# Optimization experiments

Measured on AMD Instinct MI355X. Metric: run time of the kernel, lower is better.

Reference implementation:

```python
import jax, jax.numpy as jnp
import numpy as np

MARKET_DIM, VELOCITY_DIM, AGENT_STATE_DIM = 20, 10, 10
RUNNER_DIM, POSITION_DIM, MAX_RUNNERS = 24, 8, 30
RUNNER_INPUT_DIM = RUNNER_DIM + POSITION_DIM            # 32
MARKET_TOTAL_DIM = MARKET_DIM + VELOCITY_DIM + AGENT_STATE_DIM  # 40
OBS_DIM = MARKET_DIM + VELOCITY_DIM + MAX_RUNNERS * RUNNER_DIM + AGENT_STATE_DIM + MAX_RUNNERS * POSITION_DIM  # 1000
TD_IDX = MARKET_DIM + (VELOCITY_DIM - 4)                # 26
B, T = 256, 64
MLP_H, LSTM_H = 128, 256
LSTM_IN = MLP_H + 2 * MLP_H                             # 384


def setup_inputs() -> dict:
    key = jax.random.key(0)
    ks = jax.random.split(key, 32)

    def w(k, o, i):
        return (jax.random.normal(k, (o, i), jnp.float32) / np.sqrt(i)).astype(jnp.float32)

    z = lambda n: jnp.zeros((n,), jnp.float32)
    return dict(
        obs=jax.random.normal(ks[0], (B, T, OBS_DIM), jnp.float32),
        # runner encoder: 32 -> 128 -> 128 -> 128
        re_w0=w(ks[1], MLP_H, RUNNER_INPUT_DIM), re_b0=z(MLP_H),
        re_w1=w(ks[2], MLP_H, MLP_H), re_b1=z(MLP_H),
        re_w2=w(ks[3], MLP_H, MLP_H), re_b2=z(MLP_H),
        # market encoder: 40 -> 128 -> 128 -> 128
        me_w0=w(ks[4], MLP_H, MARKET_TOTAL_DIM), me_b0=z(MLP_H),
        me_w1=w(ks[5], MLP_H, MLP_H), me_b1=z(MLP_H),
        me_w2=w(ks[6], MLP_H, MLP_H), me_b2=z(MLP_H),
        # TimeLSTM cell (single layer)
        W_ih=w(ks[7], 4 * LSTM_H, LSTM_IN), b_ih=z(4 * LSTM_H),
        W_hh=w(ks[8], 4 * LSTM_H, LSTM_H),
        W_dt=jnp.zeros((LSTM_H,), jnp.float32),
        # actor head: 384 -> 128 -> 2
        a_w0=w(ks[9], MLP_H, MLP_H + LSTM_H), a_b0=z(MLP_H),
        a_w1=w(ks[10], 2, MLP_H) * 0.01, a_b1=z(2),
        # critic head: 256 -> 128 -> 1
        c_w0=w(ks[11], MLP_H, LSTM_H), c_b0=z(MLP_H),
        c_w1=w(ks[12], 1, MLP_H), c_b1=z(1),
        log_std=jnp.zeros((MAX_RUNNERS * 2,), jnp.float32),
    )


def _mlp3(x, w0, b0, w1, b1, w2, b2):
    x = jax.nn.relu(x @ w0.T + b0)
    x = jax.nn.relu(x @ w1.T + b1)
    return x @ w2.T + b2


def _mlp2(x, w0, b0, w1, b1):
    return jax.nn.relu(x @ w0.T + b0) @ w1.T + b1


def reference(obs,
              re_w0, re_b0, re_w1, re_b1, re_w2, re_b2,
              me_w0, me_b0, me_w1, me_b1, me_w2, me_b2,
              W_ih, b_ih, W_hh, W_dt,
              a_w0, a_b0, a_w1, a_b1,
              c_w0, c_b0, c_w1, c_b1,
              log_std):
    b, t, _ = obs.shape
    of = obs.reshape(b * t, -1)
    market = of[:, :MARKET_DIM]
    vel = of[:, MARKET_DIM:MARKET_DIM + VELOCITY_DIM]
    rs = MARKET_DIM + VELOCITY_DIM
    re_ = rs + MAX_RUNNERS * RUNNER_DIM
    runners = of[:, rs:re_].reshape(b * t, MAX_RUNNERS, RUNNER_DIM)
    agent = of[:, re_:re_ + AGENT_STATE_DIM]
    ps = re_ + AGENT_STATE_DIM
    pos = of[:, ps:ps + MAX_RUNNERS * POSITION_DIM].reshape(b * t, MAX_RUNNERS, POSITION_DIM)

    market_feats = jnp.concatenate([market, vel, agent], axis=-1)        # (BT, 40)
    runner_feats = jnp.concatenate([runners, pos], axis=-1)              # (BT, R, 32)

    market_emb = _mlp3(market_feats, me_w0, me_b0, me_w1, me_b1, me_w2, me_b2)  # (BT, 128)
    runner_embs = _mlp3(runner_feats, re_w0, re_b0, re_w1, re_b1, re_w2, re_b2)  # (BT, R, 128)
    r_mean = runner_embs.mean(axis=1)
    r_max = runner_embs.max(axis=1)

    lstm_in = jnp.concatenate([market_emb, r_mean, r_max], axis=-1).reshape(b, t, LSTM_IN)
    dt = of[:, TD_IDX].reshape(b, t)

    h0 = jnp.zeros((b, LSTM_H), obs.dtype)
    c0 = jnp.zeros_like(h0)

    def step(hc, xs):
        h, c = hc
        x, d = xs                                           # (B, 384), (B,)
        gates = x @ W_ih.T + b_ih + h @ W_hh.T              # (B, 4H)
        i, f, g, o = jnp.split(gates, 4, axis=-1)
        f = f + W_dt * d[:, None]                           # time-modulated forget gate
        i, f, o = jax.nn.sigmoid(i), jax.nn.sigmoid(f), jax.nn.sigmoid(o)
        g = jnp.tanh(g)
        c_new = f * c + i * g
        h_new = o * jnp.tanh(c_new)
        return (h_new, c_new), None

    (h, c), _ = jax.lax.scan(step, (h0, c0), (lstm_in.transpose(1, 0, 2), dt.T))
    lstm_out = h  # layer_norm disabled -> identity

    runner_last = runner_embs.reshape(b, t, MAX_RUNNERS, MLP_H)[:, -1]   # (B, R, 128)
    actor_in = jnp.concatenate(
        [runner_last, jnp.broadcast_to(lstm_out[:, None, :], (b, MAX_RUNNERS, LSTM_H))], axis=-1)
    action_mean = _mlp2(actor_in, a_w0, a_b0, a_w1, a_b1).reshape(b, MAX_RUNNERS * 2)
    action_log_std = jnp.broadcast_to(log_std, action_mean.shape)
    value = _mlp2(lstm_out, c_w0, c_b0, c_w1, c_b1)                      # (B, 1)
    return action_mean, action_log_std, value, h, c
```

## Files before the change

### kernel.cpp

```cpp
#include <hip/hip_runtime.h>
#include <hip/hip_bf16.h>
#include <math.h>

#define Bn 256
#define Tn 64
#define OBSD 1000
#define NR 30
#define HD 128
#define LH 256
#define LIN 384
#define TDI 26

#define AM_OFF 0
#define ALS_OFF 15360
#define V_OFF 30720
#define H_OFF 30976
#define C_OFF 96512

typedef unsigned short u16;
typedef short bf16x8 __attribute__((ext_vector_type(8)));
typedef float f32x4 __attribute__((ext_vector_type(4)));

__device__ __forceinline__ float sigm(float x){ return 1.f/(1.f+__expf(-x)); }
__device__ __forceinline__ float tanhfast(float x){
    float ax = fabsf(x);
    float e = __expf(2.f*ax);
    float t = 1.f - 2.f/(e+1.f);
    return copysignf(t, x);
}

__device__ __forceinline__ u16 f2b(float f){
    union { __hip_bfloat16 h; u16 u; } cv;
    cv.h = __float2bfloat16(f);
    return cv.u;
}

__device__ __forceinline__ bf16x8 ld_b128_sys(const u16* p){
    bf16x8 r;
    asm volatile("global_load_dwordx4 %0, %1, off sc0 sc1"
                 : "=v"(r) : "v"(p) : "memory");
    return r;
}
__device__ __forceinline__ void st_b16_sys(u16* p, unsigned v){
    asm volatile("global_store_short %0, %1, off sc0 sc1"
                 :: "v"(p), "v"(v) : "memory");
}

#define MFMA(a,b,c) __builtin_amdgcn_mfma_f32_16x16x32_bf16(a,b,c,0,0,0)

__device__ __forceinline__ void pack_one(
    const float* __restrict__ src, u16* __restrict__ dst,
    int N, int K, int Kpad, int t)
{
    if (t >= N*Kpad) return;
    int j = t / Kpad, k = t - j*Kpad;
    float v = (k < K) ? src[j*K + k] : 0.f;
    int ntile = j>>4, jr = j&15, kc = k>>5, ko = k&31;
    int lane = ((ko>>3)<<4) | jr, elem = ko&7;
    int KC = Kpad>>5;
    dst[(size_t)(((ntile*KC + kc)*64) + lane)*8 + elem] = f2b(v);
}

__device__ __forceinline__ void pack_gi_one(
    const float* __restrict__ src, u16* __restrict__ dst, int K, int t)
{
    int KC = K >> 5;
    if (t >= 1024*K) return;
    int n = t / K, k = t - n*K;
    int nt = n>>4, jr = n&15;
    int jg = nt>>2, g = nt&3;
    float v = src[(size_t)(g*256 + jg*16 + jr)*K + k];
    int kc = k>>5, ko = k&31;
    int lane = ((ko>>3)<<4) | jr, e = ko&7;
    dst[(size_t)(((nt*KC + kc)*64) + lane)*8 + e] = f2b(v);
}

__global__ __launch_bounds__(256) void k_setup(
    const float* __restrict__ re_w0, u16* __restrict__ pw0,
    const float* __restrict__ re_w1, u16* __restrict__ pw1,
    const float* __restrict__ re_w2, u16* __restrict__ pw2,
    const float* __restrict__ me_w0, u16* __restrict__ pm0,
    const float* __restrict__ me_w1, u16* __restrict__ pm1,
    const float* __restrict__ me_w2, u16* __restrict__ pm2,
    const float* __restrict__ W_ih,  u16* __restrict__ pwih,
    const float* __restrict__ W_hh,  u16* __restrict__ pwhh,
    const float* __restrict__ obs,   float* __restrict__ dtv)
{
    int blk = blockIdx.x, tid = threadIdx.x;
    if (blk < 16){            pack_one(re_w0, pw0, 128, 32, 32,  blk*256 + tid); }
    else if (blk < 80){       pack_one(re_w1, pw1, 128,128,128, (blk-16)*256 + tid); }
    else if (blk < 144){      pack_one(re_w2, pw2, 128,128,128, (blk-80)*256 + tid); }
    else if (blk < 176){      pack_one(me_w0, pm0, 128, 40, 64, (blk-144)*256 + tid); }
    else if (blk < 240){      pack_one(me_w1, pm1, 128,128,128, (blk-176)*256 + tid); }
    else if (blk < 304){      pack_one(me_w2, pm2, 128,128,128, (blk-240)*256 + tid); }
    else if (blk < 1840){     pack_gi_one(W_ih, pwih, 384, (blk-304)*256 + tid); }
    else if (blk < 2864){     pack_gi_one(W_hh, pwhh, 256, (blk-1840)*256 + tid); }
    else {
        int idx = (blk-2864)*256 + tid;
        int b = idx >> 6, t = idx & 63;
        dtv[t*256 + b] = obs[(size_t)idx*OBSD + TDI];
    }
}

__global__ __launch_bounds__(256) void k_embed_market(
    const float* __restrict__ obs,
    const u16* __restrict__ pw0, const float* __restrict__ re_b0,
    const u16* __restrict__ pw1, const float* __restrict__ re_b1,
    const u16* __restrict__ pw2, const float* __restrict__ re_b2,
    const u16* __restrict__ pm0, const float* __restrict__ me_b0,
    const u16* __restrict__ pm1, const float* __restrict__ me_b1,
    const u16* __restrict__ pm2, const float* __restrict__ me_b2,
    u16* __restrict__ li_bf, float* __restrict__ runner_last)
{
    __shared__ __align__(16) u16 smem[19968];
    __shared__ float bsf[384];

    int blk = blockIdx.x, tid = threadIdx.x;
    int lane = tid & 63, wv = tid >> 6;
    int lr = lane & 15, lk = lane >> 4;
    f32x4 zero = {0.f,0.f,0.f,0.f};

    if (blk < 8192){
        u16* xr   = smem;
        u16* act1 = smem + 2560;
        u16* act2 = smem + 11264;
        float* bs0 = bsf, *bs1 = bsf+128, *bs2 = bsf+256;

        int bt0 = blk*2;

        for (int idx=tid; idx<2048; idx+=256){
            int r = idx>>5, k = idx&31;
            int sb = r>>5, rr = r&31;
            const float* row = obs + (size_t)(bt0+sb)*OBSD;
            float v = 0.f;
            if (rr < 30) v = (k<24) ? row[30 + rr*24 + k] : row[760 + rr*8 + (k-24)];
            xr[r*40 + k] = f2b(v);
        }
        if (tid < 128){ bs0[tid]=re_b0[tid]; bs1[tid]=re_b1[tid]; bs2[tid]=re_b2[tid]; }
        __syncthreads();

        f32x4 d[4][2];

        {
            bf16x8 a0[4];
            #pragma unroll
            for (int m=0;m<4;m++) a0[m] = *(const bf16x8*)(xr + (m*16+lr)*40 + lk*8);
            #pragma unroll
            for (int ns=0; ns<2; ns++){
                int n = 2*wv + ns;
                bf16x8 b = *(const bf16x8*)(pw0 + (size_t)(n*64 + lane)*8);
                #pragma unroll
                for (int m=0;m<4;m++) d[m][ns] = MFMA(a0[m], b, zero);
            }
        }
        #pragma unroll
        for (int m=0;m<4;m++)
            #pragma unroll
            for (int ns=0;ns<2;ns++){
                int col = (2*wv+ns)*16 + lr;
                float bias = bs0[col];
                #pragma unroll
                for (int r=0;r<4;r++)
                    act1[(m*16+lk*4+r)*136 + col] = f2b(fmaxf(d[m][ns][r] + bias, 0.f));
            }
        __syncthreads();

        #pragma unroll
        for (int m=0;m<4;m++)
            #pragma unroll
            for (int ns=0;ns<2;ns++) d[m][ns] = zero;
        #pragma unroll
        for (int kc=0; kc<4; kc++){
            bf16x8 am[4];
            #pragma unroll
            for (int m=0;m<4;m++) am[m] = *(const bf16x8*)(act1 + (m*16+lr)*136 + kc*32 + lk*8);
            #pragma unroll
            for (int ns=0; ns<2; ns++){
                int n = 2*wv + ns;
                bf16x8 b = *(const bf16x8*)(pw1 + (size_t)((n*4 + kc)*64 + lane)*8);
                #pragma unroll
                for (int m=0;m<4;m++) d[m][ns] = MFMA(am[m], b, d[m][ns]);
            }
        }
        #pragma unroll
        for (int m=0;m<4;m++)
            #pragma unroll
            for (int ns=0;ns<2;ns++){
                int col = (2*wv+ns)*16 + lr;
                float bias = bs1[col];
                #pragma unroll
                for (int r=0;r<4;r++)
                    act2[(m*16+lk*4+r)*136 + col] = f2b(fmaxf(d[m][ns][r] + bias, 0.f));
            }
        __syncthreads();

        #pragma unroll
        for (int m=0;m<4;m++)
            #pragma unroll
            for (int ns=0;ns<2;ns++) d[m][ns] = zero;
        #pragma unroll
        for (int kc=0; kc<4; kc++){
            bf16x8 am[4];
            #pragma unroll
            for (int m=0;m<4;m++) am[m] = *(const bf16x8*)(act2 + (m*16+lr)*136 + kc*32 + lk*8);
            #pragma unroll
            for (int ns=0; ns<2; ns++){
                int n = 2*wv + ns;
                bf16x8 b = *(const bf16x8*)(pw2 + (size_t)((n*4 + kc)*64 + lane)*8);
                #pragma unroll
                for (int m=0;m<4;m++) d[m][ns] = MFMA(am[m], b, d[m][ns]);
            }
        }

        u16* li0 = li_bf + (size_t)bt0*LIN;
        u16* li1 = li_bf + (size_t)(bt0+1)*LIN;
        bool last1 = (((bt0+1) & 63) == 63);
        int bb1 = (bt0+1) >> 6;

        #pragma unroll
        for (int ns=0; ns<2; ns++){
            int col = (2*wv+ns)*16 + lr;
            float bias = bs2[col];
            float vals[4][4];
            float s0=0.f, m0=-3.4e38f, s1=0.f, m1=-3.4e38f;
            #pragma unroll
            for (int m=0;m<4;m++)
                #pragma unroll
                for (int r=0;r<4;r++){
                    int rw = m*16 + lk*4 + r;
                    float v = d[m][ns][r] + bias;
                    vals[m][r] = v;
                    if (m < 2){
                        bool ok = rw < 30;
                        s0 += ok ? v : 0.f;
                        m0 = fmaxf(m0, ok ? v : -3.4e38f);
                    } else {
                        bool ok = (rw-32) < 30;
                        s1 += ok ? v : 0.f;
                        m1 = fmaxf(m1, ok ? v : -3.4e38f);
                    }
                }
            s0 += __shfl_xor(s0, 16); s0 += __shfl_xor(s0, 32);
            m0 = fmaxf(m0, __shfl_xor(m0, 16)); m0 = fmaxf(m0, __shfl_xor(m0, 32));
            s1 += __shfl_xor(s1, 16); s1 += __shfl_xor(s1, 32);
            m1 = fmaxf(m1, __shfl_xor(m1, 16)); m1 = fmaxf(m1, __shfl_xor(m1, 32));
            if (lk == 0){
                li0[128 + col] = f2b(s0 * (1.0f/30.0f));
                li0[256 + col] = f2b(m0);
            }
            if (lk == 1){
                li1[128 + col] = f2b(s1 * (1.0f/30.0f));
                li1[256 + col] = f2b(m1);
            }
            if (last1){
                #pragma unroll
                for (int m=2;m<4;m++)
                    #pragma unroll
                    for (int r=0;r<4;r++){
                        int rw = m*16 + lk*4 + r - 32;
                        if (rw < 30) runner_last[(size_t)bb1*3840 + rw*128 + col] = vals[m][r];
                    }
            }
        }
    } else {
        u16* xm  = smem;
        u16* ma1 = smem + 2304;
        u16* ma2 = smem + 6656;
        float* bs0 = bsf, *bs1 = bsf+128, *bs2 = bsf+256;

        int bt0 = (blk - 8192)*32;
        for (int idx=tid; idx<2048; idx+=256){
            int r = idx>>6, k = idx&63;
            const float* row = obs + (size_t)(bt0+r)*OBSD;
            float v = 0.f;
            if (k < 30) v = row[k];
            else if (k < 40) v = row[720 + k];
            xm[r*72 + k] = f2b(v);
        }
        if (tid < 128){ bs0[tid]=me_b0[tid]; bs1[tid]=me_b1[tid]; bs2[tid]=me_b2[tid]; }
        __syncthreads();

        f32x4 d[2][2];

        #pragma unroll
        for (int m=0;m<2;m++)
            #pragma unroll
            for (int ns=0;ns<2;ns++) d[m][ns] = zero;
        #pragma unroll
        for (int kc=0; kc<2; kc++){
            bf16x8 a0 = *(const bf16x8*)(xm + lr*72      + kc*32 + lk*8);
            bf16x8 a1 = *(const bf16x8*)(xm + (16+lr)*72 + kc*32 + lk*8);
            #pragma unroll
            for (int ns=0; ns<2; ns++){
                int n = 2*wv + ns;
                bf16x8 b = *(const bf16x8*)(pm0 + (size_t)((n*2 + kc)*64 + lane)*8);
                d[0][ns] = MFMA(a0, b, d[0][ns]);
                d[1][ns] = MFMA(a1, b, d[1][ns]);
            }
        }
        #pragma unroll
        for (int m=0;m<2;m++)
            #pragma unroll
            for (int ns=0;ns<2;ns++){
                int col = (2*wv+ns)*16 + lr;
                float bias = bs0[col];
                #pragma unroll
                for (int r=0;r<4;r++){
                    int rw = m*16 + lk*4 + r;
                    ma1[rw*136 + col] = f2b(fmaxf(d[m][ns][r] + bias, 0.f));
                }
            }
        __syncthreads();

        #pragma unroll
        for (int m=0;m<2;m++)
            #pragma unroll
            for (int ns=0;ns<2;ns++) d[m][ns] = zero;
        #pragma unroll
        for (int kc=0; kc<4; kc++){
            bf16x8 a0 = *(const bf16x8*)(ma1 + lr*136      + kc*32 + lk*8);
            bf16x8 a1 = *(const bf16x8*)(ma1 + (16+lr)*136 + kc*32 + lk*8);
            #pragma unroll
            for (int ns=0; ns<2; ns++){
                int n = 2*wv + ns;
                bf16x8 b = *(const bf16x8*)(pm1 + (size_t)((n*4 + kc)*64 + lane)*8);
                d[0][ns] = MFMA(a0, b, d[0][ns]);
                d[1][ns] = MFMA(a1, b, d[1][ns]);
            }
        }
        #pragma unroll
        for (int m=0;m<2;m++)
            #pragma unroll
            for (int ns=0;ns<2;ns++){
                int col = (2*wv+ns)*16 + lr;
                float bias = bs1[col];
                #pragma unroll
                for (int r=0;r<4;r++){
                    int rw = m*16 + lk*4 + r;
                    ma2[rw*136 + col] = f2b(fmaxf(d[m][ns][r] + bias, 0.f));
                }
            }
        __syncthreads();

        #pragma unroll
        for (int m=0;m<2;m++)
            #pragma unroll
            for (int ns=0;ns<2;ns++) d[m][ns] = zero;
        #pragma unroll
        for (int kc=0; kc<4; kc++){
            bf16x8 a0 = *(const bf16x8*)(ma2 + lr*136      + kc*32 + lk*8);
            bf16x8 a1 = *(const bf16x8*)(ma2 + (16+lr)*136 + kc*32 + lk*8);
            #pragma unroll
            for (int ns=0; ns<2; ns++){
                int n = 2*wv + ns;
                bf16x8 b = *(const bf16x8*)(pm2 + (size_t)((n*4 + kc)*64 + lane)*8);
                d[0][ns] = MFMA(a0, b, d[0][ns]);
                d[1][ns] = MFMA(a1, b, d[1][ns]);
            }
        }
        #pragma unroll
        for (int m=0;m<2;m++)
            #pragma unroll
            for (int ns=0;ns<2;ns++){
                int col = (2*wv+ns)*16 + lr;
                float bias = bs2[col];
                #pragma unroll
                for (int r=0;r<4;r++){
                    int rw = m*16 + lk*4 + r;
                    li_bf[(size_t)(bt0+rw)*LIN + col] = f2b(d[m][ns][r] + bias);
                }
            }
    }
}

__global__ __launch_bounds__(256) void k_xw(
    const u16* __restrict__ A, const u16* __restrict__ pwih,
    const float* __restrict__ b_ih, float* __restrict__ xw)
{
    __shared__ __align__(16) u16 bsh[48*512];

    int tid = threadIdx.x;
    int lane = tid & 63, wv = tid >> 6;
    int lr = lane & 15, lk = lane >> 4;
    int r0 = blockIdx.x*128 + wv*32;

    bf16x8 a[2][12];
    #pragma unroll
    for (int m=0;m<2;m++)
        #pragma unroll
        for (int kc=0;kc<12;kc++)
            a[m][kc] = *(const bf16x8*)(A + (size_t)(r0+m*16+lr)*384 + kc*32 + lk*8);

    for (int jg=0; jg<16; jg++){
        {
            const bf16x8* src = (const bf16x8*)(pwih + (size_t)jg*48*512);
            bf16x8* dst = (bf16x8*)bsh;
            #pragma unroll
            for (int i=0;i<12;i++)
                dst[tid + i*256] = src[tid + i*256];
        }
        __syncthreads();

        f32x4 acc[2][4];
        #pragma unroll
        for (int g=0; g<4; g++){
            float bias = b_ih[g*256 + jg*16 + lr];
            f32x4 v = {bias,bias,bias,bias};
            acc[0][g]=v; acc[1][g]=v;
        }
        #pragma unroll
        for (int kc=0; kc<12; kc++){
            bf16x8 b0 = *(const bf16x8*)(bsh + (size_t)((0*12+kc)*64+lane)*8);
            bf16x8 b1 = *(const bf16x8*)(bsh + (size_t)((1*12+kc)*64+lane)*8);
            bf16x8 b2 = *(const bf16x8*)(bsh + (size_t)((2*12+kc)*64+lane)*8);
            bf16x8 b3 = *(const bf16x8*)(bsh + (size_t)((3*12+kc)*64+lane)*8);
            #pragma unroll
            for (int m=0;m<2;m++){
                acc[m][0] = MFMA(a[m][kc], b0, acc[m][0]);
                acc[m][1] = MFMA(a[m][kc], b1, acc[m][1]);
                acc[m][2] = MFMA(a[m][kc], b2, acc[m][2]);
                acc[m][3] = MFMA(a[m][kc], b3, acc[m][3]);
            }
        }
        #pragma unroll
        for (int m=0;m<2;m++)
            #pragma unroll
            for (int r=0;r<4;r++){
                int row = r0 + m*16 + lk*4 + r;
                int trow = (row & 63)*256 + (row >> 6);
                float4 pk;
                pk.x = acc[m][0][r]; pk.y = acc[m][1][r];
                pk.z = acc[m][2][r]; pk.w = acc[m][3][r];
                *(float4*)(xw + ((size_t)trow*256 + jg*16 + lr)*4) = pk;
            }
        __syncthreads();
    }
}

__global__ __launch_bounds__(256,1) void k_lstm_pair(
    const float* __restrict__ xw, const u16* __restrict__ pwhh,
    const float* __restrict__ W_dt, const float* __restrict__ dtv,
    u16* __restrict__ hb0, u16* __restrict__ hb1,
    float* __restrict__ hout, float* __restrict__ cout,
    unsigned int* __restrict__ flags)
{
    int tid = threadIdx.x;
    int lane = tid & 63, wv = tid >> 6;
    int lr = lane & 15, lk = lane >> 4;
    int blk = blockIdx.x;
    int p = blk >> 1, hf = blk & 1;
    int bb0 = p*16;
    int jg0 = hf*8 + wv*2;

    bf16x8 bfr[2][4][8];
    #pragma unroll
    for (int jl=0;jl<2;jl++)
        #pragma unroll
        for (int g=0;g<4;g++)
            #pragma unroll
            for (int kc=0;kc<8;kc++)
                bfr[jl][g][kc] = *(const bf16x8*)(pwhh + (size_t)((((jg0+jl)*4+g)*8+kc)*64+lane)*8);

    float wdt0 = W_dt[jg0*16 + lr];
    float wdt1 = W_dt[(jg0+1)*16 + lr];

    float cst[2][4] = {{0.f,0.f,0.f,0.f},{0.f,0.f,0.f,0.f}};
    bf16x8 a[8];
    #pragma unroll
    for (int kc=0;kc<8;kc++) a[kc] = (bf16x8)(short)0;

    int bth = bb0 + lk*4;

    float4 xwn[2][4];
    #pragma unroll
    for (int jl=0;jl<2;jl++)
        #pragma unroll
        for (int r=0;r<4;r++)
            xwn[jl][r] = *(const float4*)(xw + ((size_t)(bth+r)*256 + (jg0+jl)*16 + lr)*4);
    float4 dtn = *(const float4*)(dtv + bth);

    unsigned int* myflag   = &flags[blk*64];
    unsigned int* partflag = &flags[(blk^1)*64];

    for (int t=0; t<64; t++){
        asm volatile("s_waitcnt vmcnt(0)" ::: "memory");
        __builtin_amdgcn_sched_barrier(0);

        f32x4 acc[2][4];
        #pragma unroll
        for (int jl=0;jl<2;jl++){
            f32x4 v0, v1, v2, v3;
            #pragma unroll
            for (int r=0;r<4;r++){
                v0[r] = xwn[jl][r].x; v1[r] = xwn[jl][r].y;
                v2[r] = xwn[jl][r].z; v3[r] = xwn[jl][r].w;
            }
            acc[jl][0] = v0; acc[jl][1] = v1; acc[jl][2] = v2; acc[jl][3] = v3;
        }

        #pragma unroll
        for (int kc=0; kc<8; kc++){
            #pragma unroll
            for (int jl=0;jl<2;jl++){
                acc[jl][0] = MFMA(a[kc], bfr[jl][0][kc], acc[jl][0]);
                acc[jl][1] = MFMA(a[kc], bfr[jl][1][kc], acc[jl][1]);
                acc[jl][2] = MFMA(a[kc], bfr[jl][2][kc], acc[jl][2]);
                acc[jl][3] = MFMA(a[kc], bfr[jl][3][kc], acc[jl][3]);
            }
        }

        u16* hw = (t&1) ? hb1 : hb0;
        #pragma unroll
        for (int jl=0;jl<2;jl++){
            float wdt = jl ? wdt1 : wdt0;
            int jcol = (jg0+jl)*16 + lr;
            #pragma unroll
            for (int r=0;r<4;r++){
                float dd = (r==0)?dtn.x:(r==1)?dtn.y:(r==2)?dtn.z:dtn.w;
                float gi = sigm(acc[jl][0][r]);
                float gf = sigm(acc[jl][1][r] + wdt*dd);
                float gg = tanhfast(acc[jl][2][r]);
                float go = sigm(acc[jl][3][r]);
                float cn = fmaf(gf, cst[jl][r], gi*gg);
                cst[jl][r] = cn;
                float hv = go * tanhfast(cn);
                if (t < 63){
                    st_b16_sys(hw + (size_t)(bth+r)*256 + jcol, (unsigned)f2b(hv));
                } else {
                    hout[(size_t)(bth+r)*256 + jcol] = hv;
                    cout[(size_t)(bth+r)*256 + jcol] = cn;
                }
            }
        }

        if (t < 63){
            asm volatile("s_waitcnt vmcnt(0)" ::: "memory");
            __syncthreads();
            if (tid == 0)
                __hip_atomic_store(myflag, (unsigned)(t+1),
                                   __ATOMIC_RELAXED, __HIP_MEMORY_SCOPE_SYSTEM);

            #pragma unroll
            for (int jl=0;jl<2;jl++)
                #pragma unroll
                for (int r=0;r<4;r++)
                    xwn[jl][r] = *(const float4*)(xw + ((size_t)((t+1)*256 + bth+r)*256 + (jg0+jl)*16 + lr)*4);
            dtn = *(const float4*)(dtv + (t+1)*256 + bth);

            if (lane == 0){
                while (__hip_atomic_load(partflag, __ATOMIC_RELAXED,
                                         __HIP_MEMORY_SCOPE_SYSTEM) < (unsigned)(t+1)) {}
            }
            __builtin_amdgcn_wave_barrier();

            const u16* hr = (t&1) ? hb1 : hb0;
            #pragma unroll
            for (int kc=0; kc<8; kc++)
                a[kc] = ld_b128_sys(hr + (size_t)(bb0+lr)*256 + kc*32 + lk*8);
        }
    }
}

__device__ __forceinline__ void dense30(
    const float* in, int istride,
    const float* __restrict__ W, int wstride, int K,
    const float* __restrict__ bias, const float* extra,
    float* outp, int ostride, bool relu, int j, int rh)
{
    float acc[15];
    #pragma unroll
    for (int i=0;i<15;i++) acc[i]=0.f;
    const float* w = W + j*wstride;
    for (int k=0;k<K;k+=4){
        float4 wv = *(const float4*)(w+k);
        #pragma unroll
        for (int i=0;i<15;i++){
            float4 xv = *(const float4*)(in + (rh+2*i)*istride + k);
            acc[i] = fmaf(wv.x,xv.x,acc[i]);
            acc[i] = fmaf(wv.y,xv.y,acc[i]);
            acc[i] = fmaf(wv.z,xv.z,acc[i]);
            acc[i] = fmaf(wv.w,xv.w,acc[i]);
        }
    }
    float bb = bias[j] + (extra ? extra[j] : 0.f);
    #pragma unroll
    for (int i=0;i<15;i++){
        float v = acc[i]+bb;
        outp[(rh+2*i)*ostride+j] = relu ? fmaxf(v,0.f) : v;
    }
}

__device__ __forceinline__ float dense1(
    const float* in, const float* __restrict__ W,
    const float* __restrict__ bias, int K, int j)
{
    const float* w = W + j*K;
    float s = 0.f;
    for (int k=0;k<K;k+=4){
        float4 wv = *(const float4*)(w+k);
        float4 xv = *(const float4*)(in+k);
        s = fmaf(wv.x,xv.x,s); s = fmaf(wv.y,xv.y,s);
        s = fmaf(wv.z,xv.z,s); s = fmaf(wv.w,xv.w,s);
    }
    return s + bias[j];
}

__global__ __launch_bounds__(256) void k_heads(
    const float* __restrict__ h, const float* __restrict__ cbuf,
    const float* __restrict__ rl,
    const float* __restrict__ a_w0, const float* __restrict__ a_b0,
    const float* __restrict__ a_w1, const float* __restrict__ a_b1,
    const float* __restrict__ c_w0, const float* __restrict__ c_b0,
    const float* __restrict__ c_w1, const float* __restrict__ c_b1,
    const float* __restrict__ log_std,
    float* __restrict__ out)
{
    __shared__ __align__(16) float hv[LH];
    __shared__ __align__(16) float rls[NR][HD];
    __shared__ __align__(16) float hid[NR][HD];
    __shared__ __align__(16) float dot2[HD];
    __shared__ __align__(16) float red[128];

    int b = blockIdx.x, tid = threadIdx.x;
    hv[tid] = h[b*LH + tid];
    for (int idx=tid; idx<NR*HD; idx+=256) rls[idx>>7][idx&127] = rl[(size_t)b*NR*HD + idx];
    __syncthreads();

    if (tid < 128){
        const float* w = a_w0 + tid*LIN + HD;
        float s = 0.f;
        for (int k=0;k<LH;k+=4){
            float4 wv = *(const float4*)(w+k);
            s = fmaf(wv.x,hv[k],s); s = fmaf(wv.y,hv[k+1],s);
            s = fmaf(wv.z,hv[k+2],s); s = fmaf(wv.w,hv[k+3],s);
        }
        dot2[tid] = s;
    }
    __syncthreads();

    int j = tid & 127, rh = tid >> 7;
    dense30(&rls[0][0], HD, a_w0, LIN, HD, a_b0, dot2, &hid[0][0], HD, true, j, rh);
    __syncthreads();

    if (tid < 60){
        int r = tid >> 1, o = tid & 1;
        const float* w = a_w1 + o*HD;
        float s = a_b1[o];
        for (int k=0;k<HD;k++) s = fmaf(hid[r][k], w[k], s);
        out[AM_OFF + b*60 + tid] = s;
        out[ALS_OFF + b*60 + tid] = log_std[tid];
    }

    float term = 0.f;
    if (tid < 128) term = fmaxf(dense1(hv, c_w0, c_b0, LH, tid), 0.f) * c_w1[tid];
    if (tid < 128) red[tid] = term;
    __syncthreads();
    for (int s2=64; s2>0; s2>>=1){
        if (tid < s2) red[tid] += red[tid+s2];
        __syncthreads();
    }
    if (tid == 0) out[V_OFF + b] = red[0] + c_b1[0];

    out[H_OFF + b*LH + tid] = hv[tid];
    out[C_OFF + b*LH + tid] = cbuf[b*LH + tid];
}

extern "C" void kernel_launch(void* const* d_in, const int* in_sizes, int n_in,
                              void* d_out, int out_size, void* d_ws, size_t ws_size,
                              hipStream_t stream)
{
    const float* obs   = (const float*)d_in[0];
    const float* re_w0 = (const float*)d_in[1];
    const float* re_b0 = (const float*)d_in[2];
    const float* re_w1 = (const float*)d_in[3];
    const float* re_b1 = (const float*)d_in[4];
    const float* re_w2 = (const float*)d_in[5];
    const float* re_b2 = (const float*)d_in[6];
    const float* me_w0 = (const float*)d_in[7];
    const float* me_b0 = (const float*)d_in[8];
    const float* me_w1 = (const float*)d_in[9];
    const float* me_b1 = (const float*)d_in[10];
    const float* me_w2 = (const float*)d_in[11];
    const float* me_b2 = (const float*)d_in[12];
    const float* W_ih  = (const float*)d_in[13];
    const float* b_ih  = (const float*)d_in[14];
    const float* W_hh  = (const float*)d_in[15];
    const float* W_dt  = (const float*)d_in[16];
    const float* a_w0  = (const float*)d_in[17];
    const float* a_b0  = (const float*)d_in[18];
    const float* a_w1  = (const float*)d_in[19];
    const float* a_b1  = (const float*)d_in[20];
    const float* c_w0  = (const float*)d_in[21];
    const float* c_b0  = (const float*)d_in[22];
    const float* c_w1  = (const float*)d_in[23];
    const float* c_b1  = (const float*)d_in[24];
    const float* lstd  = (const float*)d_in[25];
    float* out = (float*)d_out;

    float* ws = (float*)d_ws;
    size_t off = 0;
    float* xw4  = ws + off; off += (size_t)16384*1024;
    float* hout = ws + off; off += (size_t)Bn*LH;
    float* cb   = ws + off; off += (size_t)Bn*LH;
    float* rl   = ws + off; off += (size_t)Bn*NR*HD;
    float* dtv  = ws + off; off += (size_t)16384;
    unsigned int* flags = (unsigned int*)(ws + off); off += 2048;

    u16* us = (u16*)(ws + off);
    size_t uo = 0;
    u16* li_bf = us + uo; uo += (size_t)16384*LIN;
    u16* pw0   = us + uo; uo += 128*32;
    u16* pw1   = us + uo; uo += 128*128;
    u16* pw2   = us + uo; uo += 128*128;
    u16* pm0   = us + uo; uo += 128*64;
    u16* pm1   = us + uo; uo += 128*128;
    u16* pm2   = us + uo; uo += 128*128;
    u16* pwih  = us + uo; uo += (size_t)1024*384;
    u16* pwhh  = us + uo; uo += (size_t)1024*256;
    u16* hb0   = us + uo; uo += (size_t)Bn*LH;
    u16* hb1   = us + uo; uo += (size_t)Bn*LH;

    hipMemsetAsync(flags, 0, 2048*sizeof(unsigned int), stream);

    k_setup<<<2928, 256, 0, stream>>>(re_w0, pw0, re_w1, pw1, re_w2, pw2,
                                      me_w0, pm0, me_w1, pm1, me_w2, pm2,
                                      W_ih, pwih, W_hh, pwhh, obs, dtv);

    k_embed_market<<<8704, 256, 0, stream>>>(obs,
                                      pw0, re_b0, pw1, re_b1, pw2, re_b2,
                                      pm0, me_b0, pm1, me_b1, pm2, me_b2,
                                      li_bf, rl);

    k_xw<<<128, 256, 0, stream>>>(li_bf, pwih, b_ih, xw4);

    k_lstm_pair<<<32, 256, 0, stream>>>(xw4, pwhh, W_dt, dtv, hb0, hb1,
                                        hout, cb, flags);

    k_heads<<<256, 256, 0, stream>>>(hout, cb, rl,
        a_w0, a_b0, a_w1, a_b1, c_w0, c_b0, c_w1, c_b1, lstd, out);
}
```

Measured before the change: 456.1 us.

## Process four timesteps per runner-embed block, fold flag reset into setup, hoist LSTM acc init

Each runner-encoder block now handles four (b,t) rows instead of two, halving the block count and reusing each weight fragment load across twice as many MFMAs. A single activation buffer is reused across layers, with an extra barrier added. The flag memset is folded into the setup kernel to drop one launch. In the LSTM loop, accumulator initialization from the prefetched xw values moves to the end of the previous iteration so it is off the critical path. The cost is higher register and LDS use per block, which may reduce occupancy.

Measured after the change: 464.6 us. About the same (+1.9%).

```diff
diff --git a/kernel.cpp b/kernel.cpp
--- a/kernel.cpp
+++ b/kernel.cpp
@@ -84,7 +84,8 @@
     const float* __restrict__ me_w2, u16* __restrict__ pm2,
     const float* __restrict__ W_ih,  u16* __restrict__ pwih,
     const float* __restrict__ W_hh,  u16* __restrict__ pwhh,
-    const float* __restrict__ obs,   float* __restrict__ dtv)
+    const float* __restrict__ obs,   float* __restrict__ dtv,
+    unsigned int* __restrict__ flags)
 {
     int blk = blockIdx.x, tid = threadIdx.x;
     if (blk < 16){            pack_one(re_w0, pw0, 128, 32, 32,  blk*256 + tid); }
@@ -95,10 +96,12 @@
     else if (blk < 304){      pack_one(me_w2, pm2, 128,128,128, (blk-240)*256 + tid); }
     else if (blk < 1840){     pack_gi_one(W_ih, pwih, 384, (blk-304)*256 + tid); }
     else if (blk < 2864){     pack_gi_one(W_hh, pwhh, 256, (blk-1840)*256 + tid); }
-    else {
+    else if (blk < 2928){
         int idx = (blk-2864)*256 + tid;
         int b = idx >> 6, t = idx & 63;
         dtv[t*256 + b] = obs[(size_t)idx*OBSD + TDI];
+    } else {
+        flags[(blk-2928)*256 + tid] = 0u;
     }
 }
 
@@ -112,7 +115,7 @@
     const u16* __restrict__ pm2, const float* __restrict__ me_b2,
     u16* __restrict__ li_bf, float* __restrict__ runner_last)
 {
-    __shared__ __align__(16) u16 smem[19968];
+    __shared__ __align__(16) u16 smem[22528];
     __shared__ float bsf[384];
 
     int blk = blockIdx.x, tid = threadIdx.x;
@@ -120,15 +123,14 @@
     int lr = lane & 15, lk = lane >> 4;
     f32x4 zero = {0.f,0.f,0.f,0.f};
 
-    if (blk < 8192){
-        u16* xr   = smem;
-        u16* act1 = smem + 2560;
-        u16* act2 = smem + 11264;
+    if (blk < 4096){
+        u16* xr  = smem;
+        u16* act = smem + 5120;
         float* bs0 = bsf, *bs1 = bsf+128, *bs2 = bsf+256;
 
-        int bt0 = blk*2;
-
-        for (int idx=tid; idx<2048; idx+=256){
+        int bt0 = blk*4;
+
+        for (int idx=tid; idx<4096; idx+=256){
             int r = idx>>5, k = idx&31;
             int sb = r>>5, rr = r&31;
             const float* row = obs + (size_t)(bt0+sb)*OBSD;
@@ -139,126 +141,138 @@
         if (tid < 128){ bs0[tid]=re_b0[tid]; bs1[tid]=re_b1[tid]; bs2[tid]=re_b2[tid]; }
         __syncthreads();
 
-        f32x4 d[4][2];
+        f32x4 d[8][2];
 
         {
-            bf16x8 a0[4];
-            #pragma unroll
-            for (int m=0;m<4;m++) a0[m] = *(const bf16x8*)(xr + (m*16+lr)*40 + lk*8);
+            bf16x8 a0[8];
+            #pragma unroll
+            for (int m=0;m<8;m++) a0[m] = *(const bf16x8*)(xr + (m*16+lr)*40 + lk*8);
             #pragma unroll
             for (int ns=0; ns<2; ns++){
                 int n = 2*wv + ns;
                 bf16x8 b = *(const bf16x8*)(pw0 + (size_t)(n*64 + lane)*8);
                 #pragma unroll
-                for (int m=0;m<4;m++) d[m][ns] = MFMA(a0[m], b, zero);
-            }
-        }
-        #pragma unroll
-        for (int m=0;m<4;m++)
+                for (int m=0;m<8;m++) d[m][ns] = MFMA(a0[m], b, zero);
+            }
+        }
+        #pragma unroll
+        for (int m=0;m<8;m++)
             #pragma unroll
             for (int ns=0;ns<2;ns++){
                 int col = (2*wv+ns)*16 + lr;
                 float bias = bs0[col];
                 #pragma unroll
                 for (int r=0;r<4;r++)
-                    act1[(m*16+lk*4+r)*136 + col] = f2b(fmaxf(d[m][ns][r] + bias, 0.f));
-            }
-        __syncthreads();
-
-        #pragma unroll
-        for (int m=0;m<4;m++)
+                    act[(m*16+lk*4+r)*136 + col] = f2b(fmaxf(d[m][ns][r] + bias, 0.f));
+            }
+        __syncthreads();
+
+        #pragma unroll
+        for (int m=0;m<8;m++)
             #pragma unroll
             for (int ns=0;ns<2;ns++) d[m][ns] = zero;
         #pragma unroll
         for (int kc=0; kc<4; kc++){
-            bf16x8 am[4];
-            #pragma unroll
-            for (int m=0;m<4;m++) am[m] = *(const bf16x8*)(act1 + (m*16+lr)*136 + kc*32 + lk*8);
+            bf16x8 am[8];
+            #pragma unroll
+            for (int m=0;m<8;m++) am[m] = *(const bf16x8*)(act + (m*16+lr)*136 + kc*32 + lk*8);
             #pragma unroll
             for (int ns=0; ns<2; ns++){
                 int n = 2*wv + ns;
                 bf16x8 b = *(const bf16x8*)(pw1 + (size_t)((n*4 + kc)*64 + lane)*8);
                 #pragma unroll
-                for (int m=0;m<4;m++) d[m][ns] = MFMA(am[m], b, d[m][ns]);
-            }
-        }
-        #pragma unroll
-        for (int m=0;m<4;m++)
+                for (int m=0;m<8;m++) d[m][ns] = MFMA(am[m], b, d[m][ns]);
+            }
+        }
+        __syncthreads();
+        #pragma unroll
+        for (int m=0;m<8;m++)
             #pragma unroll
             for (int ns=0;ns<2;ns++){
                 int col = (2*wv+ns)*16 + lr;
                 float bias = bs1[col];
                 #pragma unroll
                 for (int r=0;r<4;r++)
-                    act2[(m*16+lk*4+r)*136 + col] = f2b(fmaxf(d[m][ns][r] + bias, 0.f));
-            }
-        __syncthreads();
-
-        #pragma unroll
-        for (int m=0;m<4;m++)
+                    act[(m*16+lk*4+r)*136 + col] = f2b(fmaxf(d[m][ns][r] + bias, 0.f));
+            }
+        __syncthreads();
+
+        #pragma unroll
+        for (int m=0;m<8;m++)
             #pragma unroll
             for (int ns=0;ns<2;ns++) d[m][ns] = zero;
         #pragma unroll
         for (int kc=0; kc<4; kc++){
-            bf16x8 am[4];
-            #pragma unroll
-            for (int m=0;m<4;m++) am[m] = *(const bf16x8*)(act2 + (m*16+lr)*136 + kc*32 + lk*8);
+            bf16x8 am[8];
+            #pragma unroll
+            for (int m=0;m<8;m++) am[m] = *(const bf16x8*)(act + (m*16+lr)*136 + kc*32 + lk*8);
             #pragma unroll
             for (int ns=0; ns<2; ns++){
                 int n = 2*wv + ns;
                 bf16x8 b = *(const bf16x8*)(pw2 + (size_t)((n*4 + kc)*64 + lane)*8);
                 #pragma unroll
-                for (int m=0;m<4;m++) d[m][ns] = MFMA(am[m], b, d[m][ns]);
-            }
-        }
-
-        u16* li0 = li_bf + (size_t)bt0*LIN;
-        u16* li1 = li_bf + (size_t)(bt0+1)*LIN;
-        bool last1 = (((bt0+1) & 63) == 63);
-        int bb1 = (bt0+1) >> 6;
+                for (int m=0;m<8;m++) d[m][ns] = MFMA(am[m], b, d[m][ns]);
+            }
+        }
+
+        bool last3 = (((bt0+3) & 63) == 63);
+        int bb3 = (bt0+3) >> 6;
 
         #pragma unroll
         for (int ns=0; ns<2; ns++){
             int col = (2*wv+ns)*16 + lr;
             float bias = bs2[col];
-            float vals[4][4];
-            float s0=0.f, m0=-3.4e38f, s1=0.f, m1=-3.4e38f;
-            #pragma unroll
-            for (int m=0;m<4;m++)
+            float vals[8][4];
+            float ss0=0.f, ss1=0.f, ss2=0.f, ss3=0.f;
+            float mm0=-3.4e38f, mm1=-3.4e38f, mm2=-3.4e38f, mm3=-3.4e38f;
+            #pragma unroll
+            for (int m=0;m<8;m++)
                 #pragma unroll
                 for (int r=0;r<4;r++){
                     int rw = m*16 + lk*4 + r;
                     float v = d[m][ns][r] + bias;
                     vals[m][r] = v;
-                    if (m < 2){
-                        bool ok = rw < 30;
-                        s0 += ok ? v : 0.f;
-                        m0 = fmaxf(m0, ok ? v : -3.4e38f);
-                    } else {
-                        bool ok = (rw-32) < 30;
-                        s1 += ok ? v : 0.f;
-                        m1 = fmaxf(m1, ok ? v : -3.4e38f);
-                    }
+                    int sb = m >> 1;
+                    bool ok = (rw - sb*32) < 30;
+                    float va = ok ? v : 0.f;
+                    float vm = ok ? v : -3.4e38f;
+                    if (sb == 0){ ss0 += va; mm0 = fmaxf(mm0, vm); }
+                    else if (sb == 1){ ss1 += va; mm1 = fmaxf(mm1, vm); }
+                    else if (sb == 2){ ss2 += va; mm2 = fmaxf(mm2, vm); }
+                    else { ss3 += va; mm3 = fmaxf(mm3, vm); }
                 }
-            s0 += __shfl_xor(s0, 16); s0 += __shfl_xor(s0, 32);
-            m0 = fmaxf(m0, __shfl_xor(m0, 16)); m0 = fmaxf(m0, __shfl_xor(m0, 32));
-            s1 += __shfl_xor(s1, 16); s1 += __shfl_xor(s1, 32);
-            m1 = fmaxf(m1, __shfl_xor(m1, 16)); m1 = fmaxf(m1, __shfl_xor(m1, 32));
+            ss0 += __shfl_xor(ss0, 16); ss0 += __shfl_xor(ss0, 32);
+            mm0 = fmaxf(mm0, __shfl_xor(mm0, 16)); mm0 = fmaxf(mm0, __shfl_xor(mm0, 32));
+            ss1 += __shfl_xor(ss1, 16); ss1 += __shfl_xor(ss1, 32);
+            mm1 = fmaxf(mm1, __shfl_xor(mm1, 16)); mm1 = fmaxf(mm1, __shfl_xor(mm1, 32));
+            ss2 += __shfl_xor(ss2, 16); ss2 += __shfl_xor(ss2, 32);
+            mm2 = fmaxf(mm2, __shfl_xor(mm2, 16)); mm2 = fmaxf(mm2, __shfl_xor(mm2, 32));
+            ss3 += __shfl_xor(ss3, 16); ss3 += __shfl_xor(ss3, 32);
+            mm3 = fmaxf(mm3, __shfl_xor(mm3, 16)); mm3 = fmaxf(mm3, __shfl_xor(mm3, 32));
             if (lk == 0){
-                li0[128 + col] = f2b(s0 * (1.0f/30.0f));
-                li0[256 + col] = f2b(m0);
-            }
-            if (lk == 1){
-                li1[128 + col] = f2b(s1 * (1.0f/30.0f));
-                li1[256 + col] = f2b(m1);
-            }
-            if (last1){
-                #pragma unroll
-                for (int m=2;m<4;m++)
+                u16* li = li_bf + (size_t)(bt0+0)*LIN;
+                li[128 + col] = f2b(ss0 * (1.0f/30.0f));
+                li[256 + col] = f2b(mm0);
+            } else if (lk == 1){
+                u16* li = li_bf + (size_t)(bt0+1)*LIN;
+                li[128 + col] = f2b(ss1 * (1.0f/30.0f));
+                li[256 + col] = f2b(mm1);
+            } else if (lk == 2){
+                u16* li = li_bf + (size_t)(bt0+2)*LIN;
+                li[128 + col] = f2b(ss2 * (1.0f/30.0f));
+                li[256 + col] = f2b(mm2);
+            } else {
+                u16* li = li_bf + (size_t)(bt0+3)*LIN;
+                li[128 + col] = f2b(ss3 * (1.0f/30.0f));
+                li[256 + col] = f2b(mm3);
+            }
+            if (last3){
+                #pragma unroll
+                for (int m=6;m<8;m++)
                     #pragma unroll
                     for (int r=0;r<4;r++){
-                        int rw = m*16 + lk*4 + r - 32;
-                        if (rw < 30) runner_last[(size_t)bb1*3840 + rw*128 + col] = vals[m][r];
+                        int rwl = m*16 + lk*4 + r - 96;
+                        if (rwl < 30) runner_last[(size_t)bb3*3840 + rwl*128 + col] = vals[m][r];
                     }
             }
         }
@@ -268,7 +282,7 @@
         u16* ma2 = smem + 6656;
         float* bs0 = bsf, *bs1 = bsf+128, *bs2 = bsf+256;
 
-        int bt0 = (blk - 8192)*32;
+        int bt0 = (blk - 4096)*32;
         for (int idx=tid; idx<2048; idx+=256){
             int r = idx>>6, k = idx&63;
             const float* row = obs + (size_t)(bt0+r)*OBSD;
@@ -479,24 +493,24 @@
             xwn[jl][r] = *(const float4*)(xw + ((size_t)(bth+r)*256 + (jg0+jl)*16 + lr)*4);
     float4 dtn = *(const float4*)(dtv + bth);
 
+    f32x4 acc[2][4];
+    #pragma unroll
+    for (int jl=0;jl<2;jl++){
+        f32x4 v0, v1, v2, v3;
+        #pragma unroll
+        for (int r=0;r<4;r++){
+            v0[r] = xwn[jl][r].x; v1[r] = xwn[jl][r].y;
+            v2[r] = xwn[jl][r].z; v3[r] = xwn[jl][r].w;
+        }
+        acc[jl][0] = v0; acc[jl][1] = v1; acc[jl][2] = v2; acc[jl][3] = v3;
+    }
+
     unsigned int* myflag   = &flags[blk*64];
     unsigned int* partflag = &flags[(blk^1)*64];
 
     for (int t=0; t<64; t++){
         asm volatile("s_waitcnt vmcnt(0)" ::: "memory");
         __builtin_amdgcn_sched_barrier(0);
-
-        f32x4 acc[2][4];
-        #pragma unroll
-        for (int jl=0;jl<2;jl++){
-            f32x4 v0, v1, v2, v3;
-            #pragma unroll
-            for (int r=0;r<4;r++){
-                v0[r] = xwn[jl][r].x; v1[r] = xwn[jl][r].y;
-                v2[r] = xwn[jl][r].z; v3[r] = xwn[jl][r].w;
-            }
-            acc[jl][0] = v0; acc[jl][1] = v1; acc[jl][2] = v2; acc[jl][3] = v3;
-        }
 
         #pragma unroll
         for (int kc=0; kc<8; kc++){
@@ -557,6 +571,17 @@
             #pragma unroll
             for (int kc=0; kc<8; kc++)
                 a[kc] = ld_b128_sys(hr + (size_t)(bb0+lr)*256 + kc*32 + lk*8);
+
+            #pragma unroll
+            for (int jl=0;jl<2;jl++){
+                f32x4 v0, v1, v2, v3;
+                #pragma unroll
+                for (int r=0;r<4;r++){
+                    v0[r] = xwn[jl][r].x; v1[r] = xwn[jl][r].y;
+                    v2[r] = xwn[jl][r].z; v3[r] = xwn[jl][r].w;
+                }
+                acc[jl][0] = v0; acc[jl][1] = v1; acc[jl][2] = v2; acc[jl][3] = v3;
+            }
         }
     }
 }
@@ -720,13 +745,11 @@
     u16* hb0   = us + uo; uo += (size_t)Bn*LH;
     u16* hb1   = us + uo; uo += (size_t)Bn*LH;
 
-    hipMemsetAsync(flags, 0, 2048*sizeof(unsigned int), stream);
-
-    k_setup<<<2928, 256, 0, stream>>>(re_w0, pw0, re_w1, pw1, re_w2, pw2,
+    k_setup<<<2936, 256, 0, stream>>>(re_w0, pw0, re_w1, pw1, re_w2, pw2,
                                       me_w0, pm0, me_w1, pm1, me_w2, pm2,
-                                      W_ih, pwih, W_hh, pwhh, obs, dtv);
-
-    k_embed_market<<<8704, 256, 0, stream>>>(obs,
+                                      W_ih, pwih, W_hh, pwhh, obs, dtv, flags);
+
+    k_embed_market<<<4608, 256, 0, stream>>>(obs,
                                       pw0, re_b0, pw1, re_b1, pw2, re_b2,
                                       pm0, me_b0, pm1, me_b1, pm2, me_b2,
                                       li_bf, rl);
```
